# Optimization experiments

Measured on AMD Instinct MI355X. Metric: run time of the kernel, lower is better.

Reference implementation:

```python
import jax, jax.numpy as jnp
import numpy as np

B, T, C = 2, 2048, 2048
H, HK = 16, 4
HD = C // H
N_REP = H // HK


def setup_inputs() -> dict:
    key = jax.random.key(0)
    ks = jax.random.split(key, 10)
    sc_in = 1.0 / np.sqrt(C)
    x = jax.random.normal(ks[0], (B, T, C), dtype=jnp.float32)
    # rotary embeddings (realistic cos/sin from inv_freq)
    inv_freq = 1.0 / (10000.0 ** (jnp.arange(0, HD, 2, dtype=jnp.float32) / HD))
    freqs = jnp.arange(T, dtype=jnp.float32)[:, None] * inv_freq[None, :]  # [T, HD/2]
    emb = jnp.concatenate([freqs, freqs], axis=-1)  # [T, HD]
    cos = jnp.broadcast_to(jnp.cos(emb)[None], (B, T, HD))
    sin = jnp.broadcast_to(jnp.sin(emb)[None], (B, T, HD))
    Wq = jax.random.normal(ks[1], (C, H * HD), dtype=jnp.float32) * sc_in
    bq = jnp.zeros((H * HD,), dtype=jnp.float32)
    Wk = jax.random.normal(ks[2], (C, HK * HD), dtype=jnp.float32) * sc_in
    bk = jnp.zeros((HK * HD,), dtype=jnp.float32)
    Wv = jax.random.normal(ks[3], (C, HK * HD), dtype=jnp.float32) * sc_in
    bv = jnp.zeros((HK * HD,), dtype=jnp.float32)
    Wo = jax.random.normal(ks[4], (C, C), dtype=jnp.float32) * sc_in
    return {"x": x, "cos": cos, "sin": sin, "Wq": Wq, "bq": bq,
            "Wk": Wk, "bk": bk, "Wv": Wv, "bv": bv, "Wo": Wo}


def _rotate_half(t):
    t1, t2 = jnp.split(t, 2, axis=-1)
    return jnp.concatenate([-t2, t1], axis=-1)


def reference(x, cos, sin, Wq, bq, Wk, bk, Wv, bv, Wo):
    b, t, c = x.shape
    q = (x @ Wq + bq).reshape(b, t, H, HD).transpose(0, 2, 1, 3)   # [B,H,T,HD]
    k = (x @ Wk + bk).reshape(b, t, HK, HD).transpose(0, 2, 1, 3)  # [B,HK,T,HD]
    v = (x @ Wv + bv).reshape(b, t, HK, HD).transpose(0, 2, 1, 3)  # [B,HK,T,HD]
    co = cos[:, None, :, :]  # [B,1,T,HD]
    si = sin[:, None, :, :]
    q = q * co + _rotate_half(q) * si
    k = k * co + _rotate_half(k) * si
    # GQA without materializing repeated K/V: group query heads per KV head
    qg = q.reshape(b, HK, N_REP, t, HD)
    scale = 1.0 / np.sqrt(HD)
    scores = jnp.einsum('bgrqd,bgkd->bgrqk', qg, k) * scale  # [B,HK,n_rep,T,T]
    causal = jnp.tril(jnp.ones((t, t), dtype=bool))
    scores = jnp.where(causal, scores, jnp.finfo(scores.dtype).min)
    att = jax.nn.softmax(scores, axis=-1)
    yg = jnp.einsum('bgrqk,bgkd->bgrqd', att, v)  # [B,HK,n_rep,T,HD]
    y = yg.reshape(b, H, t, HD).transpose(0, 2, 1, 3).reshape(b, t, c)
    return y @ Wo
```

## Files before the change

kernel.cpp:

```cpp
#include <hip/hip_runtime.h>
#include <math.h>

#define BB 2
#define TT 2048
#define CC 2048
#define HH 16
#define HKK 4
#define HD 128
#define MM (BB*TT)

typedef short bf16x8 __attribute__((ext_vector_type(8)));
typedef float f32x4 __attribute__((ext_vector_type(4)));

#define GLOBAL_AS(p) ((const __attribute__((address_space(1))) void*)(p))
#define LDS_AS(p)    ((__attribute__((address_space(3))) void*)(p))

__device__ __forceinline__ unsigned short f2bf(float f) {
    unsigned u = __float_as_uint(f);
    u += 0x7fff + ((u >> 16) & 1);
    return (unsigned short)(u >> 16);
}
__device__ __forceinline__ float bf2f(unsigned short h) {
    return __uint_as_float(((unsigned)h) << 16);
}

#define QSCALE (0.08838834764831845f * 1.44269504088896340736f)

__global__ __launch_bounds__(256) void cast_x_kernel(
    const float* __restrict__ x, unsigned short* __restrict__ xb)
{
    size_t i = ((size_t)blockIdx.x * 256 + threadIdx.x) * 8;
    float4 a = *(const float4*)&x[i];
    float4 b = *(const float4*)&x[i + 4];
    uint4 r;
    r.x = f2bf(a.x) | ((unsigned)f2bf(a.y) << 16);
    r.y = f2bf(a.z) | ((unsigned)f2bf(a.w) << 16);
    r.z = f2bf(b.x) | ((unsigned)f2bf(b.y) << 16);
    r.w = f2bf(b.z) | ((unsigned)f2bf(b.w) << 16);
    *(uint4*)&xb[i] = r;
}

__global__ __launch_bounds__(256) void wtrans_kernel(
    const float* __restrict__ Wq, const float* __restrict__ Wk,
    const float* __restrict__ Wv, const float* __restrict__ Wo,
    unsigned short* __restrict__ Wt, unsigned short* __restrict__ Wot)
{
    __shared__ float tile[64][65];
    int z = blockIdx.z;
    const float* src; unsigned short* dst; int ldW, nmax, noff;
    if (z == 0)      { src = Wq; dst = Wt;  ldW = 2048; nmax = 2048; noff = 0; }
    else if (z == 1) { src = Wk; dst = Wt;  ldW = 512;  nmax = 512;  noff = 2048; }
    else if (z == 2) { src = Wv; dst = Wt;  ldW = 512;  nmax = 512;  noff = 2560; }
    else             { src = Wo; dst = Wot; ldW = 2048; nmax = 2048; noff = 0; }
    int n0 = blockIdx.y * 64;
    if (n0 >= nmax) return;
    int k0 = blockIdx.x * 64;
    int tx = threadIdx.x & 15, ty = threadIdx.x >> 4;
#pragma unroll
    for (int i = 0; i < 4; ++i) {
        int r = ty + i * 16;
        float4 v4 = *(const float4*)&src[(size_t)(k0 + r) * ldW + n0 + tx * 4];
        tile[r][tx * 4 + 0] = v4.x;
        tile[r][tx * 4 + 1] = v4.y;
        tile[r][tx * 4 + 2] = v4.z;
        tile[r][tx * 4 + 3] = v4.w;
    }
    __syncthreads();
#pragma unroll
    for (int i = 0; i < 4; ++i) {
        int r = ty + i * 16;
        int c = tx * 4;
        ushort4 o;
        o.x = f2bf(tile[c + 0][r]);
        o.y = f2bf(tile[c + 1][r]);
        o.z = f2bf(tile[c + 2][r]);
        o.w = f2bf(tile[c + 3][r]);
        *(ushort4*)&dst[(size_t)(noff + n0 + r) * 2048 + k0 + c] = o;
    }
}

__device__ __forceinline__ void gemm_core_128x128x64(
    const unsigned short* __restrict__ A, const unsigned short* __restrict__ B,
    short* As, short* Bs, int m0, int n0,
    const int* mrow, const int* nrow, f32x4 (&acc)[4][4])
{
    const int tid = threadIdx.x;
    const int lane = tid & 63;
    const int w = tid >> 6;
    const int lm = lane & 15;
    const int q8 = lane >> 4;
    const int lrow = lane >> 3;
    const int lchunk = lane & 7;

    for (int kt = 0; kt < CC; kt += 64) {
        __syncthreads();
#pragma unroll
        for (int jj = 0; jj < 4; ++jj) {
            int rA = w * 32 + jj * 8 + lrow;
            int cA = ((lchunk ^ (rA & 7)) << 3);
            __builtin_amdgcn_global_load_lds(
                GLOBAL_AS(&A[(size_t)(m0 + rA) * CC + kt + cA]),
                LDS_AS(&As[(w * 32 + jj * 8) * 64]), 16, 0, 0);
            __builtin_amdgcn_global_load_lds(
                GLOBAL_AS(&B[(size_t)(n0 + rA) * CC + kt + cA]),
                LDS_AS(&Bs[(w * 32 + jj * 8) * 64]), 16, 0, 0);
        }
        __syncthreads();
#pragma unroll
        for (int ksi = 0; ksi < 2; ++ksi) {
            bf16x8 af[4], bfr[4];
#pragma unroll
            for (int i = 0; i < 4; ++i) {
                int xo = (((ksi * 4 + q8) ^ (lm & 7)) << 3);
                af[i]  = *(const bf16x8*)&As[(mrow[i] + lm) * 64 + xo];
                bfr[i] = *(const bf16x8*)&Bs[(nrow[i] + lm) * 64 + xo];
            }
#pragma unroll
            for (int im = 0; im < 4; ++im)
#pragma unroll
                for (int in = 0; in < 4; ++in)
                    acc[im][in] = __builtin_amdgcn_mfma_f32_16x16x32_bf16(af[im], bfr[in], acc[im][in], 0, 0, 0);
        }
    }
}

__global__ __launch_bounds__(256, 3) void qkv_gemm_mfma(
    const unsigned short* __restrict__ xb, const unsigned short* __restrict__ Wt,
    const float* __restrict__ bq, const float* __restrict__ bk, const float* __restrict__ bv,
    const float* __restrict__ cosb, const float* __restrict__ sinb,
    unsigned short* __restrict__ q, unsigned short* __restrict__ k, unsigned short* __restrict__ v)
{
    __shared__ __attribute__((aligned(16))) short As[128 * 64];
    __shared__ __attribute__((aligned(16))) short Bs[128 * 64];
    const int lane = threadIdx.x & 63;
    const int w = threadIdx.x >> 6;
    const int w1 = w >> 1;
    const int m0 = blockIdx.y * 128;
    const int n0 = blockIdx.x * 128;
    const int lm = lane & 15;
    const int q8 = lane >> 4;

    int mrow[4], nrow[4];
#pragma unroll
    for (int i = 0; i < 4; ++i) {
        mrow[i] = (w & 1) * 64 + i * 16;
        nrow[i] = w1 * 32 + (i & 1) * 16 + (i >> 1) * 64;
    }

    f32x4 acc[4][4];
#pragma unroll
    for (int im = 0; im < 4; ++im)
#pragma unroll
        for (int in = 0; in < 4; ++in) acc[im][in] = {0.f, 0.f, 0.f, 0.f};

    gemm_core_128x128x64(xb, Wt, As, Bs, m0, n0, mrow, nrow, acc);

    unsigned short* dst; const float* bias; int ldD, off, mode;
    if (n0 < 2048)      { dst = q; bias = bq; ldD = 2048; off = n0;        mode = 0; }
    else if (n0 < 2560) { dst = k; bias = bk; ldD = 512;  off = n0 - 2048; mode = 1; }
    else                { dst = v; bias = bv; ldD = 512;  off = n0 - 2560; mode = 2; }

    float bv_[4];
#pragma unroll
    for (int in = 0; in < 4; ++in) bv_[in] = bias[off + nrow[in] + lm];

#pragma unroll
    for (int im = 0; im < 4; ++im) {
        int rowbase = m0 + mrow[im] + q8 * 4;
        float t[4][4];
#pragma unroll
        for (int in = 0; in < 4; ++in)
#pragma unroll
            for (int r = 0; r < 4; ++r) t[in][r] = acc[im][in][r] + bv_[in];
        if (mode < 2) {
#pragma unroll
            for (int in = 0; in < 4; ++in) {
                int d = nrow[in] + lm;
                float sgn = (in < 2) ? -1.f : 1.f;
#pragma unroll
                for (int r = 0; r < 4; ++r) {
                    int row = rowbase + r;
                    float c = cosb[row * HD + d];
                    float s = sinb[row * HD + d];
                    float o = c * t[in][r] + sgn * s * t[in ^ 2][r];
                    if (mode == 0) o *= QSCALE;
                    dst[(size_t)row * ldD + off + d] = f2bf(o);
                }
            }
        } else {
#pragma unroll
            for (int in = 0; in < 4; ++in)
#pragma unroll
                for (int r = 0; r < 4; ++r)
                    dst[(size_t)(rowbase + r) * ldD + off + nrow[in] + lm] = f2bf(t[in][r]);
        }
    }
}

__global__ __launch_bounds__(256, 3) void out_gemm_mfma(
    const unsigned short* __restrict__ yb, const unsigned short* __restrict__ Wot,
    float* __restrict__ Cout)
{
    __shared__ __attribute__((aligned(16))) short As[128 * 64];
    __shared__ __attribute__((aligned(16))) short Bs[128 * 64];
    const int lane = threadIdx.x & 63;
    const int w = threadIdx.x >> 6;
    const int m0 = blockIdx.y * 128;
    const int n0 = blockIdx.x * 128;
    const int lm = lane & 15;
    const int q8 = lane >> 4;

    int mrow[4], nrow[4];
#pragma unroll
    for (int i = 0; i < 4; ++i) {
        mrow[i] = (w & 1) * 64 + i * 16;
        nrow[i] = (w >> 1) * 64 + i * 16;
    }

    f32x4 acc[4][4];
#pragma unroll
    for (int im = 0; im < 4; ++im)
#pragma unroll
        for (int in = 0; in < 4; ++in) acc[im][in] = {0.f, 0.f, 0.f, 0.f};

    gemm_core_128x128x64(yb, Wot, As, Bs, m0, n0, mrow, nrow, acc);

#pragma unroll
    for (int im = 0; im < 4; ++im)
#pragma unroll
        for (int in = 0; in < 4; ++in)
#pragma unroll
            for (int r = 0; r < 4; ++r) {
                int row = m0 + mrow[im] + q8 * 4 + r;
                Cout[(size_t)row * CC + n0 + nrow[in] + lm] = acc[im][in][r];
            }
}

__global__ __launch_bounds__(256) void vtrans_kernel(
    const unsigned short* __restrict__ v, unsigned short* __restrict__ vt)
{
    __shared__ unsigned short tile[64][68];
    int bg = blockIdx.z;
    int b = bg >> 2, g = bg & 3;
    int t0 = blockIdx.x * 64;
    int d0 = blockIdx.y * 64;
    int tx = threadIdx.x & 15, ty = threadIdx.x >> 4;
#pragma unroll
    for (int i = 0; i < 4; ++i) {
        int r = ty + i * 16;
        ushort4 v4 = *(const ushort4*)&v[(size_t)(b * TT + t0 + r) * (HKK * HD) + g * HD + d0 + tx * 4];
        tile[r][tx * 4 + 0] = v4.x;
        tile[r][tx * 4 + 1] = v4.y;
        tile[r][tx * 4 + 2] = v4.z;
        tile[r][tx * 4 + 3] = v4.w;
    }
    __syncthreads();
#pragma unroll
    for (int i = 0; i < 4; ++i) {
        int r = ty + i * 16;
        int c = tx * 4;
        ushort4 o;
        o.x = tile[c + 0][r];
        o.y = tile[c + 1][r];
        o.z = tile[c + 2][r];
        o.w = tile[c + 3][r];
        *(ushort4*)&vt[(size_t)(bg * HD + d0 + r) * TT + t0 + c] = o;
    }
}

static __device__ const signed char QI_T[24] = {
    15, 7, 14, 14, 13, 6, 12, 11,
    15, 13, 12, 10, 10, 9, 11, 5,
    0, 1, 2, 3, 8, 4, 8, 9
};
static __device__ const signed char HF_T[24] = {
    0, 2, 0, 1, 1, 2, 1, 1,
    1, 0, 0, 0, 1, 0, 0, 2,
    2, 2, 2, 2, 0, 2, 1, 1
};

__global__ __launch_bounds__(512, 4) void flash_mfma(
    const unsigned short* __restrict__ q, const unsigned short* __restrict__ k,
    const unsigned short* __restrict__ vt, unsigned short* __restrict__ y,
    float* __restrict__ po, float* __restrict__ sb)
{
    __shared__ __attribute__((aligned(16))) short SM[26624];
    short* Ks = SM;
    short* Vs = SM + 8704;
    short* Ps = SM + 17920;

    const int tid = threadIdx.x;
    const int lane = tid & 63;
    const int w = tid >> 6;
    const int lm = lane & 15;
    const int q8 = lane >> 4;
    const int bh = blockIdx.x;
    const int b = bh >> 4, h = bh & 15, g = h >> 2;
    const int yb_ = blockIdx.y;
    const int qi = QI_T[yb_];
    const int hf = HF_T[yb_];
    const int q0 = qi * 128;
    const int wrow = w * 16;
    const int jdiag = 2 * qi + (w >> 2);
    int j0, jend;
    if (hf == 2)      { j0 = 0;      jend = 2 * qi + 2; }
    else if (hf == 0) { j0 = 0;      jend = qi + 1; }
    else              { j0 = qi + 1; jend = 2 * qi + 2; }

    bf16x8 qf[4];
#pragma unroll
    for (int ks = 0; ks < 4; ++ks)
        qf[ks] = *(const bf16x8*)&q[(size_t)(b * TT + q0 + wrow + lm) * CC
                                    + h * HD + ks * 32 + q8 * 8];

    f32x4 o_acc[8];
#pragma unroll
    for (int nt = 0; nt < 8; ++nt) o_acc[nt] = {0.f, 0.f, 0.f, 0.f};
    float m_i = -1e30f;
    float l_i = 0.f;

    int ktok[2], ke8[2], vd[2], vt8[2];
#pragma unroll
    for (int i = 0; i < 2; ++i) {
        int f = tid + i * 512;
        ktok[i] = f >> 4; ke8[i] = (f & 15) * 8;
        vd[i]   = f >> 3; vt8[i] = (f & 7) * 8;
    }
    const unsigned short* kbase = k + (size_t)(b * TT) * (HKK * HD) + g * HD;
    const unsigned short* vbase = vt + (size_t)((b * 4 + g) * HD) * TT;

    uint4 kreg[2], vreg[2];
#pragma unroll
    for (int i = 0; i < 2; ++i) {
        kreg[i] = *(const uint4*)&kbase[(size_t)(j0 * 64 + ktok[i]) * (HKK * HD) + ke8[i]];
        vreg[i] = *(const uint4*)&vbase[(size_t)vd[i] * TT + j0 * 64 + vt8[i]];
    }

    short* Pw = Ps + w * 16 * 68;
    const int mrow = (w & 3) * 16 + lm;

    for (int j = j0; j < jend; ++j) {
        __syncthreads();
#pragma unroll
        for (int i = 0; i < 2; ++i) {
            *(uint4*)&Ks[ktok[i] * 136 + ke8[i]] = kreg[i];
            *(uint4*)&Vs[vd[i] * 72 + vt8[i]]    = vreg[i];
        }
        __syncthreads();
        if (j + 1 < jend) {
#pragma unroll
            for (int i = 0; i < 2; ++i) {
                kreg[i] = *(const uint4*)&kbase[(size_t)((j + 1) * 64 + ktok[i]) * (HKK * HD) + ke8[i]];
                vreg[i] = *(const uint4*)&vbase[(size_t)vd[i] * TT + (j + 1) * 64 + vt8[i]];
            }
        }

        if (j <= jdiag) {
            f32x4 sacc[4];
#pragma unroll
            for (int ct = 0; ct < 4; ++ct) {
                sacc[ct] = {0.f, 0.f, 0.f, 0.f};
#pragma unroll
                for (int ks = 0; ks < 4; ++ks) {
                    bf16x8 kf = *(const bf16x8*)&Ks[(ct * 16 + lm) * 136 + ks * 32 + q8 * 8];
                    sacc[ct] = __builtin_amdgcn_mfma_f32_16x16x32_bf16(kf, qf[ks], sacc[ct], 0, 0, 0);
                }
            }
            if (j == jdiag) {
#pragma unroll
                for (int ct = 0; ct < 4; ++ct)
#pragma unroll
                    for (int r = 0; r < 4; ++r)
                        if (ct * 16 + q8 * 4 + r > mrow) sacc[ct][r] = -1e30f;
            }
            float tmax = fmaxf(
                fmaxf(fmaxf(fmaxf(sacc[0][0], sacc[0][1]), fmaxf(sacc[0][2], sacc[0][3])),
                      fmaxf(fmaxf(sacc[1][0], sacc[1][1]), fmaxf(sacc[1][2], sacc[1][3]))),
                fmaxf(fmaxf(fmaxf(sacc[2][0], sacc[2][1]), fmaxf(sacc[2][2], sacc[2][3])),
                      fmaxf(fmaxf(sacc[3][0], sacc[3][1]), fmaxf(sacc[3][2], sacc[3][3]))));
            tmax = fmaxf(tmax, __shfl_xor(tmax, 16));
            tmax = fmaxf(tmax, __shfl_xor(tmax, 32));
            float m_new = fmaxf(m_i, tmax);
            float alpha = exp2f(m_i - m_new);
            m_i = m_new;

            float ps = 0.f;
#pragma unroll
            for (int ct = 0; ct < 4; ++ct) {
                ushort4 pp;
                float p0 = exp2f(sacc[ct][0] - m_new);
                float p1 = exp2f(sacc[ct][1] - m_new);
                float p2 = exp2f(sacc[ct][2] - m_new);
                float p3 = exp2f(sacc[ct][3] - m_new);
                ps += (p0 + p1) + (p2 + p3);
                pp.x = f2bf(p0); pp.y = f2bf(p1); pp.z = f2bf(p2); pp.w = f2bf(p3);
                *(ushort4*)&Pw[lm * 68 + ct * 16 + q8 * 4] = pp;
            }
            l_i = l_i * alpha + ps;

            float a0 = __shfl(alpha, q8 * 4 + 0);
            float a1 = __shfl(alpha, q8 * 4 + 1);
            float a2 = __shfl(alpha, q8 * 4 + 2);
            float a3 = __shfl(alpha, q8 * 4 + 3);
#pragma unroll
            for (int nt = 0; nt < 8; ++nt) {
                o_acc[nt][0] *= a0;
                o_acc[nt][1] *= a1;
                o_acc[nt][2] *= a2;
                o_acc[nt][3] *= a3;
            }

#pragma unroll
            for (int ks2 = 0; ks2 < 2; ++ks2) {
                bf16x8 pf = *(const bf16x8*)&Pw[lm * 68 + ks2 * 32 + q8 * 8];
#pragma unroll
                for (int nt = 0; nt < 8; ++nt) {
                    bf16x8 vf = *(const bf16x8*)&Vs[(nt * 16 + lm) * 72 + ks2 * 32 + q8 * 8];
                    o_acc[nt] = __builtin_amdgcn_mfma_f32_16x16x32_bf16(pf, vf, o_acc[nt], 0, 0, 0);
                }
            }
        }
    }

    float lf = l_i;
    lf += __shfl_xor(lf, 16);
    lf += __shfl_xor(lf, 32);
    float inv[4];
#pragma unroll
    for (int r = 0; r < 4; ++r) inv[r] = 1.f / __shfl(lf, q8 * 4 + r);

    if (hf == 2) {
        __syncthreads();
        short* Es = SM;
#pragma unroll
        for (int nt = 0; nt < 8; ++nt)
#pragma unroll
            for (int r = 0; r < 4; ++r)
                Es[(wrow + q8 * 4 + r) * 136 + nt * 16 + lm] = (short)f2bf(o_acc[nt][r] * inv[r]);
        __syncthreads();
#pragma unroll
        for (int i = 0; i < 4; ++i) {
            int f = tid + i * 512;
            int row = f >> 4, ch = f & 15;
            uint4 t = *(const uint4*)&Es[row * 136 + ch * 8];
            *(uint4*)&y[(size_t)(b * TT + q0 + row) * CC + h * HD + ch * 8] = t;
        }
    } else {
        const int pi = ((bh << 3) + (qi - 8)) * 2 + hf;
        if (lane < 16) sb[pi * 128 + wrow + lane] = lf * exp2f(m_i);
        float* pb = po + (size_t)pi * 16384;
#pragma unroll
        for (int nt = 0; nt < 8; ++nt)
#pragma unroll
            for (int r = 0; r < 4; ++r)
                pb[(wrow + q8 * 4 + r) * 128 + nt * 16 + lm] = o_acc[nt][r] * inv[r];
    }
}

__global__ __launch_bounds__(256) void combine_kernel(
    const float* __restrict__ po, const float* __restrict__ sb,
    unsigned short* __restrict__ y)
{
    const int bh = blockIdx.x;
    const int b = bh >> 4, h = bh & 15;
    const int qi = 8 + blockIdx.y;
    const int p0 = ((bh << 3) + (qi - 8)) * 2;
    const int t = threadIdx.x;
    const int row = t >> 1, d0 = (t & 1) * 64;
    float s0 = sb[p0 * 128 + row];
    float s1 = sb[(p0 + 1) * 128 + row];
    float w0 = s0 / (s0 + s1);
    float w1 = 1.f - w0;
    const float* a = &po[(size_t)p0 * 16384 + row * 128 + d0];
    const float* c = &po[(size_t)(p0 + 1) * 16384 + row * 128 + d0];
    unsigned short* yr = &y[(size_t)(b * TT + qi * 128 + row) * CC + h * HD + d0];
#pragma unroll
    for (int i = 0; i < 64; i += 4) {
        float4 xa = *(const float4*)&a[i];
        float4 xc = *(const float4*)&c[i];
        ushort4 o;
        o.x = f2bf(w0 * xa.x + w1 * xc.x);
        o.y = f2bf(w0 * xa.y + w1 * xc.y);
        o.z = f2bf(w0 * xa.z + w1 * xc.z);
        o.w = f2bf(w0 * xa.w + w1 * xc.w);
        *(ushort4*)&yr[i] = o;
    }
}

extern "C" void kernel_launch(void* const* d_in, const int* in_sizes, int n_in,
                              void* d_out, int out_size, void* d_ws, size_t ws_size,
                              hipStream_t stream) {
    const float* x    = (const float*)d_in[0];
    const float* cosb = (const float*)d_in[1];
    const float* sinb = (const float*)d_in[2];
    const float* Wq   = (const float*)d_in[3];
    const float* bq   = (const float*)d_in[4];
    const float* Wk   = (const float*)d_in[5];
    const float* bk   = (const float*)d_in[6];
    const float* Wv   = (const float*)d_in[7];
    const float* bv   = (const float*)d_in[8];
    const float* Wo   = (const float*)d_in[9];
    float* out = (float*)d_out;

    unsigned short* xb  = (unsigned short*)d_ws;
    unsigned short* Wt  = xb  + (size_t)MM * CC;
    unsigned short* Wot = Wt  + (size_t)3072 * 2048;
    unsigned short* qb  = Wot + (size_t)2048 * 2048;
    unsigned short* kb  = qb  + (size_t)MM * CC;
    unsigned short* vb  = kb  + (size_t)MM * (HKK * HD);
    unsigned short* vtb = vb  + (size_t)MM * (HKK * HD);
    unsigned short* ybf = vtb + (size_t)BB * HKK * HD * TT;

    float* po = (float*)d_out;
    float* sbuf = (float*)xb;

    cast_x_kernel<<<dim3((MM * CC) / 2048), 256, 0, stream>>>(x, xb);
    wtrans_kernel<<<dim3(32, 32, 4), 256, 0, stream>>>(Wq, Wk, Wv, Wo, Wt, Wot);
    qkv_gemm_mfma<<<dim3(3072 / 128, MM / 128), 256, 0, stream>>>(
        xb, Wt, bq, bk, bv, cosb, sinb, qb, kb, vb);
    vtrans_kernel<<<dim3(TT / 64, HD / 64, BB * HKK), 256, 0, stream>>>(vb, vtb);
    flash_mfma<<<dim3(BB * HH, 24), 512, 0, stream>>>(qb, kb, vtb, ybf, po, sbuf);
    combine_kernel<<<dim3(BB * HH, 8), 256, 0, stream>>>(po, sbuf, ybf);
    out_gemm_mfma<<<dim3(CC / 128, MM / 128), 256, 0, stream>>>(ybf, Wot, out);
}
```

Baseline: 368.1 us.

## Switch flash attention to 32x32 MFMA with register-resident P via permlane swap

Rewrites the attention kernel to use 32x32x16 bf16 MFMA tiles, with 4 waves of 32 query rows each instead of 8 waves of 16. The softmax probabilities are packed to bf16 and rearranged in registers with permlane32 swaps, so they feed the PV MFMA directly and the LDS round-trip for P goes away. Row max and sum now need fewer cross-lane shuffles, and the alpha rescale needs no shuffles at all. In exchange, block size halves and each thread carries larger accumulators, so register pressure and occupancy change.

```diff
diff --git a/kernel.cpp b/kernel.cpp
--- a/kernel.cpp
+++ b/kernel.cpp
@@ -11,6 +11,8 @@
 
 typedef short bf16x8 __attribute__((ext_vector_type(8)));
 typedef float f32x4 __attribute__((ext_vector_type(4)));
+typedef float f32x16 __attribute__((ext_vector_type(16)));
+typedef int   i32x4 __attribute__((ext_vector_type(4)));
 
 #define GLOBAL_AS(p) ((const __attribute__((address_space(1))) void*)(p))
 #define LDS_AS(p)    ((__attribute__((address_space(3))) void*)(p))
@@ -279,181 +281,197 @@
     2, 2, 2, 2, 0, 2, 1, 1
 };
 
-__global__ __launch_bounds__(512, 4) void flash_mfma(
+__global__ __launch_bounds__(256, 2) void flash_mfma(
     const unsigned short* __restrict__ q, const unsigned short* __restrict__ k,
     const unsigned short* __restrict__ vt, unsigned short* __restrict__ y,
     float* __restrict__ po, float* __restrict__ sb)
 {
-    __shared__ __attribute__((aligned(16))) short SM[26624];
+    __shared__ __attribute__((aligned(16))) short SM[17920];
     short* Ks = SM;
     short* Vs = SM + 8704;
-    short* Ps = SM + 17920;
 
     const int tid = threadIdx.x;
     const int lane = tid & 63;
     const int w = tid >> 6;
-    const int lm = lane & 15;
-    const int q8 = lane >> 4;
+    const int l31 = lane & 31;
+    const int hi = lane >> 5;
     const int bh = blockIdx.x;
     const int b = bh >> 4, h = bh & 15, g = h >> 2;
     const int yb_ = blockIdx.y;
     const int qi = QI_T[yb_];
     const int hf = HF_T[yb_];
     const int q0 = qi * 128;
-    const int wrow = w * 16;
-    const int jdiag = 2 * qi + (w >> 2);
+    const int jdiag = 2 * qi + (w >> 1);
     int j0, jend;
     if (hf == 2)      { j0 = 0;      jend = 2 * qi + 2; }
     else if (hf == 0) { j0 = 0;      jend = qi + 1; }
     else              { j0 = qi + 1; jend = 2 * qi + 2; }
 
-    bf16x8 qf[4];
-#pragma unroll
-    for (int ks = 0; ks < 4; ++ks)
-        qf[ks] = *(const bf16x8*)&q[(size_t)(b * TT + q0 + wrow + lm) * CC
-                                    + h * HD + ks * 32 + q8 * 8];
-
-    f32x4 o_acc[8];
-#pragma unroll
-    for (int nt = 0; nt < 8; ++nt) o_acc[nt] = {0.f, 0.f, 0.f, 0.f};
+    bf16x8 qf[8];
+#pragma unroll
+    for (int ks = 0; ks < 8; ++ks)
+        qf[ks] = *(const bf16x8*)&q[(size_t)(b * TT + q0 + w * 32 + l31) * CC
+                                    + h * HD + ks * 16 + hi * 8];
+
+    f32x16 o_acc[4];
+#pragma unroll
+    for (int t = 0; t < 4; ++t)
+#pragma unroll
+        for (int e = 0; e < 16; ++e) o_acc[t][e] = 0.f;
     float m_i = -1e30f;
     float l_i = 0.f;
 
-    int ktok[2], ke8[2], vd[2], vt8[2];
-#pragma unroll
-    for (int i = 0; i < 2; ++i) {
-        int f = tid + i * 512;
+    int ktok[4], ke8[4], vd[4], vt8[4];
+#pragma unroll
+    for (int i = 0; i < 4; ++i) {
+        int f = tid + i * 256;
         ktok[i] = f >> 4; ke8[i] = (f & 15) * 8;
         vd[i]   = f >> 3; vt8[i] = (f & 7) * 8;
     }
     const unsigned short* kbase = k + (size_t)(b * TT) * (HKK * HD) + g * HD;
     const unsigned short* vbase = vt + (size_t)((b * 4 + g) * HD) * TT;
 
-    uint4 kreg[2], vreg[2];
-#pragma unroll
-    for (int i = 0; i < 2; ++i) {
+    uint4 kreg[4], vreg[4];
+#pragma unroll
+    for (int i = 0; i < 4; ++i) {
         kreg[i] = *(const uint4*)&kbase[(size_t)(j0 * 64 + ktok[i]) * (HKK * HD) + ke8[i]];
         vreg[i] = *(const uint4*)&vbase[(size_t)vd[i] * TT + j0 * 64 + vt8[i]];
     }
 
-    short* Pw = Ps + w * 16 * 68;
-    const int mrow = (w & 3) * 16 + lm;
-
     for (int j = j0; j < jend; ++j) {
         __syncthreads();
 #pragma unroll
-        for (int i = 0; i < 2; ++i) {
+        for (int i = 0; i < 4; ++i) {
             *(uint4*)&Ks[ktok[i] * 136 + ke8[i]] = kreg[i];
             *(uint4*)&Vs[vd[i] * 72 + vt8[i]]    = vreg[i];
         }
         __syncthreads();
         if (j + 1 < jend) {
 #pragma unroll
-            for (int i = 0; i < 2; ++i) {
+            for (int i = 0; i < 4; ++i) {
                 kreg[i] = *(const uint4*)&kbase[(size_t)((j + 1) * 64 + ktok[i]) * (HKK * HD) + ke8[i]];
                 vreg[i] = *(const uint4*)&vbase[(size_t)vd[i] * TT + (j + 1) * 64 + vt8[i]];
             }
         }
 
         if (j <= jdiag) {
-            f32x4 sacc[4];
-#pragma unroll
-            for (int ct = 0; ct < 4; ++ct) {
-                sacc[ct] = {0.f, 0.f, 0.f, 0.f};
-#pragma unroll
-                for (int ks = 0; ks < 4; ++ks) {
-                    bf16x8 kf = *(const bf16x8*)&Ks[(ct * 16 + lm) * 136 + ks * 32 + q8 * 8];
-                    sacc[ct] = __builtin_amdgcn_mfma_f32_16x16x32_bf16(kf, qf[ks], sacc[ct], 0, 0, 0);
+            f32x16 sacc[2];
+#pragma unroll
+            for (int ct = 0; ct < 2; ++ct) {
+#pragma unroll
+                for (int e = 0; e < 16; ++e) sacc[ct][e] = 0.f;
+#pragma unroll
+                for (int ks = 0; ks < 8; ++ks) {
+                    bf16x8 kf = *(const bf16x8*)&Ks[(ct * 32 + l31) * 136 + ks * 16 + hi * 8];
+                    sacc[ct] = __builtin_amdgcn_mfma_f32_32x32x16_bf16(kf, qf[ks], sacc[ct], 0, 0, 0);
                 }
             }
             if (j == jdiag) {
-#pragma unroll
-                for (int ct = 0; ct < 4; ++ct)
-#pragma unroll
-                    for (int r = 0; r < 4; ++r)
-                        if (ct * 16 + q8 * 4 + r > mrow) sacc[ct][r] = -1e30f;
-            }
-            float tmax = fmaxf(
-                fmaxf(fmaxf(fmaxf(sacc[0][0], sacc[0][1]), fmaxf(sacc[0][2], sacc[0][3])),
-                      fmaxf(fmaxf(sacc[1][0], sacc[1][1]), fmaxf(sacc[1][2], sacc[1][3]))),
-                fmaxf(fmaxf(fmaxf(sacc[2][0], sacc[2][1]), fmaxf(sacc[2][2], sacc[2][3])),
-                      fmaxf(fmaxf(sacc[3][0], sacc[3][1]), fmaxf(sacc[3][2], sacc[3][3]))));
-            tmax = fmaxf(tmax, __shfl_xor(tmax, 16));
+                int lim = l31 + 32 * (w & 1);
+#pragma unroll
+                for (int ct = 0; ct < 2; ++ct)
+#pragma unroll
+                    for (int reg = 0; reg < 16; ++reg) {
+                        int tok = ct * 32 + (reg & 3) + 8 * (reg >> 2) + 4 * hi;
+                        if (tok > lim) sacc[ct][reg] = -1e30f;
+                    }
+            }
+            float tmax = sacc[0][0];
+#pragma unroll
+            for (int e = 1; e < 16; ++e) tmax = fmaxf(tmax, sacc[0][e]);
+#pragma unroll
+            for (int e = 0; e < 16; ++e) tmax = fmaxf(tmax, sacc[1][e]);
             tmax = fmaxf(tmax, __shfl_xor(tmax, 32));
             float m_new = fmaxf(m_i, tmax);
             float alpha = exp2f(m_i - m_new);
             m_i = m_new;
 
+            float p[2][16];
             float ps = 0.f;
 #pragma unroll
-            for (int ct = 0; ct < 4; ++ct) {
-                ushort4 pp;
-                float p0 = exp2f(sacc[ct][0] - m_new);
-                float p1 = exp2f(sacc[ct][1] - m_new);
-                float p2 = exp2f(sacc[ct][2] - m_new);
-                float p3 = exp2f(sacc[ct][3] - m_new);
-                ps += (p0 + p1) + (p2 + p3);
-                pp.x = f2bf(p0); pp.y = f2bf(p1); pp.z = f2bf(p2); pp.w = f2bf(p3);
-                *(ushort4*)&Pw[lm * 68 + ct * 16 + q8 * 4] = pp;
-            }
+            for (int ct = 0; ct < 2; ++ct)
+#pragma unroll
+                for (int reg = 0; reg < 16; ++reg) {
+                    p[ct][reg] = exp2f(sacc[ct][reg] - m_new);
+                    ps += p[ct][reg];
+                }
             l_i = l_i * alpha + ps;
 
-            float a0 = __shfl(alpha, q8 * 4 + 0);
-            float a1 = __shfl(alpha, q8 * 4 + 1);
-            float a2 = __shfl(alpha, q8 * 4 + 2);
-            float a3 = __shfl(alpha, q8 * 4 + 3);
-#pragma unroll
-            for (int nt = 0; nt < 8; ++nt) {
-                o_acc[nt][0] *= a0;
-                o_acc[nt][1] *= a1;
-                o_acc[nt][2] *= a2;
-                o_acc[nt][3] *= a3;
-            }
-
-#pragma unroll
-            for (int ks2 = 0; ks2 < 2; ++ks2) {
-                bf16x8 pf = *(const bf16x8*)&Pw[lm * 68 + ks2 * 32 + q8 * 8];
-#pragma unroll
-                for (int nt = 0; nt < 8; ++nt) {
-                    bf16x8 vf = *(const bf16x8*)&Vs[(nt * 16 + lm) * 72 + ks2 * 32 + q8 * 8];
-                    o_acc[nt] = __builtin_amdgcn_mfma_f32_16x16x32_bf16(pf, vf, o_acc[nt], 0, 0, 0);
+#pragma unroll
+            for (int t = 0; t < 4; ++t)
+#pragma unroll
+                for (int e = 0; e < 16; ++e) o_acc[t][e] *= alpha;
+
+            int W[2][4][2];
+#pragma unroll
+            for (int ct = 0; ct < 2; ++ct)
+#pragma unroll
+                for (int bb = 0; bb < 4; ++bb)
+#pragma unroll
+                    for (int jj = 0; jj < 2; ++jj)
+                        asm("v_cvt_pk_bf16_f32 %0, %1, %2"
+                            : "=v"(W[ct][bb][jj])
+                            : "v"(p[ct][4 * bb + 2 * jj]), "v"(p[ct][4 * bb + 2 * jj + 1]));
+
+#pragma unroll
+            for (int ks = 0; ks < 4; ++ks) {
+                int a0 = W[ks >> 1][2 * (ks & 1)][0];
+                int a1 = W[ks >> 1][2 * (ks & 1)][1];
+                int b0 = W[ks >> 1][2 * (ks & 1) + 1][0];
+                int b1 = W[ks >> 1][2 * (ks & 1) + 1][1];
+                asm("v_permlane32_swap_b32 %0, %1" : "+v"(a0), "+v"(b0));
+                asm("v_permlane32_swap_b32 %0, %1" : "+v"(a1), "+v"(b1));
+                i32x4 wv; wv[0] = a0; wv[1] = a1; wv[2] = b0; wv[3] = b1;
+                bf16x8 pa = __builtin_bit_cast(bf16x8, wv);
+#pragma unroll
+                for (int t = 0; t < 4; ++t) {
+                    bf16x8 vf = *(const bf16x8*)&Vs[(t * 32 + l31) * 72 + ks * 16 + hi * 8];
+                    o_acc[t] = __builtin_amdgcn_mfma_f32_32x32x16_bf16(vf, pa, o_acc[t], 0, 0, 0);
                 }
             }
         }
     }
 
-    float lf = l_i;
-    lf += __shfl_xor(lf, 16);
-    lf += __shfl_xor(lf, 32);
-    float inv[4];
-#pragma unroll
-    for (int r = 0; r < 4; ++r) inv[r] = 1.f / __shfl(lf, q8 * 4 + r);
+    float lf = l_i + __shfl_xor(l_i, 32);
+    float invl = 1.f / lf;
 
     if (hf == 2) {
         __syncthreads();
         short* Es = SM;
 #pragma unroll
-        for (int nt = 0; nt < 8; ++nt)
-#pragma unroll
-            for (int r = 0; r < 4; ++r)
-                Es[(wrow + q8 * 4 + r) * 136 + nt * 16 + lm] = (short)f2bf(o_acc[nt][r] * inv[r]);
+        for (int t = 0; t < 4; ++t)
+#pragma unroll
+            for (int rg = 0; rg < 4; ++rg) {
+                ushort4 o;
+                o.x = f2bf(o_acc[t][rg * 4 + 0] * invl);
+                o.y = f2bf(o_acc[t][rg * 4 + 1] * invl);
+                o.z = f2bf(o_acc[t][rg * 4 + 2] * invl);
+                o.w = f2bf(o_acc[t][rg * 4 + 3] * invl);
+                *(ushort4*)&Es[(w * 32 + l31) * 136 + t * 32 + 8 * rg + 4 * hi] = o;
+            }
         __syncthreads();
 #pragma unroll
-        for (int i = 0; i < 4; ++i) {
-            int f = tid + i * 512;
+        for (int i = 0; i < 8; ++i) {
+            int f = tid + i * 256;
             int row = f >> 4, ch = f & 15;
-            uint4 t = *(const uint4*)&Es[row * 136 + ch * 8];
-            *(uint4*)&y[(size_t)(b * TT + q0 + row) * CC + h * HD + ch * 8] = t;
+            uint4 tv = *(const uint4*)&Es[row * 136 + ch * 8];
+            *(uint4*)&y[(size_t)(b * TT + q0 + row) * CC + h * HD + ch * 8] = tv;
         }
     } else {
         const int pi = ((bh << 3) + (qi - 8)) * 2 + hf;
-        if (lane < 16) sb[pi * 128 + wrow + lane] = lf * exp2f(m_i);
+        if (hi == 0) sb[pi * 128 + w * 32 + l31] = lf * exp2f(m_i);
         float* pb = po + (size_t)pi * 16384;
 #pragma unroll
-        for (int nt = 0; nt < 8; ++nt)
-#pragma unroll
-            for (int r = 0; r < 4; ++r)
-                pb[(wrow + q8 * 4 + r) * 128 + nt * 16 + lm] = o_acc[nt][r] * inv[r];
+        for (int t = 0; t < 4; ++t)
+#pragma unroll
+            for (int rg = 0; rg < 4; ++rg) {
+                float4 o;
+                o.x = o_acc[t][rg * 4 + 0] * invl;
+                o.y = o_acc[t][rg * 4 + 1] * invl;
+                o.z = o_acc[t][rg * 4 + 2] * invl;
+                o.w = o_acc[t][rg * 4 + 3] * invl;
+                *(float4*)&pb[(w * 32 + l31) * 128 + t * 32 + 8 * rg + 4 * hi] = o;
+            }
     }
 }
 
@@ -519,7 +537,7 @@
     qkv_gemm_mfma<<<dim3(3072 / 128, MM / 128), 256, 0, stream>>>(
         xb, Wt, bq, bk, bv, cosb, sinb, qb, kb, vb);
     vtrans_kernel<<<dim3(TT / 64, HD / 64, BB * HKK), 256, 0, stream>>>(vb, vtb);
-    flash_mfma<<<dim3(BB * HH, 24), 512, 0, stream>>>(qb, kb, vtb, ybf, po, sbuf);
+    flash_mfma<<<dim3(BB * HH, 24), 256, 0, stream>>>(qb, kb, vtb, ybf, po, sbuf);
     combine_kernel<<<dim3(BB * HH, 8), 256, 0, stream>>>(po, sbuf, ybf);
     out_gemm_mfma<<<dim3(CC / 128, MM / 128), 256, 0, stream>>>(ybf, Wot, out);
 }
```

After: 395.8 us. 1.08x slower.
